# Performance work log

Measured on AMD Instinct MI355X. Metric: run time of the kernel, lower is better.

Reference implementation:

```python
import jax, jax.numpy as jnp
import numpy as np

B, S, D = 2, 2048, 2048
H, HD = 16, 128


def _rope_cos_sin(seq_len, head_dim, base=10000.0):
    inv_freq = 1.0 / (base ** (np.arange(0, head_dim, 2, dtype=np.float32) / head_dim))
    t = np.arange(seq_len, dtype=np.float32)
    freqs = np.outer(t, inv_freq)                      # [S, HD/2]
    emb = np.concatenate([freqs, freqs], axis=-1)      # [S, HD]
    return jnp.asarray(np.cos(emb)), jnp.asarray(np.sin(emb))


def setup_inputs() -> dict:
    key = jax.random.key(0)
    k1, k2, k3 = jax.random.split(key, 3)
    hidden_states = jax.random.normal(k1, (B, S, D), dtype=jnp.float32)
    cos, sin = _rope_cos_sin(S, HD)
    # qkv weight: [3, H*HD, D] as in CastedLinear(batch_output_dims=(3,))
    w_qkv = jax.random.normal(k2, (3, H * HD, D), dtype=jnp.float32) * (1.0 / D ** 0.5)
    w_o = jax.random.normal(k3, (D, H * HD), dtype=jnp.float32) * (1.0 / (H * HD) ** 0.5)
    return {"hidden_states": hidden_states, "cos": cos, "sin": sin, "w_qkv": w_qkv, "w_o": w_o}


def _rotate_half(x):
    x1, x2 = jnp.split(x, 2, axis=-1)
    return jnp.concatenate([-x2, x1], axis=-1)


def _apply_rope(x, cos, sin):
    # x: [B, S, H, HD]; cos/sin: [S, HD] -> broadcast over heads via [:, None, :]
    return x * cos[:, None, :] + _rotate_half(x) * sin[:, None, :]


def reference(hidden_states, cos, sin, w_qkv, w_o):
    # fused QKV projection: weight flattened to [3*H*HD, D]
    qkv = jnp.einsum('bsd,fd->bsf', hidden_states, w_qkv.reshape(-1, D))  # [B,S,3*H*HD]
    # rearrange '... (h hd) -> ... h hd' with h=H  ->  [B,S,H,3*HD], then chunk
    qkv = qkv.reshape(B, S, H, 3 * HD)
    q, k, v = jnp.split(qkv, 3, axis=-1)          # each [B,S,H,HD]
    q = _apply_rope(q, cos, sin)
    k = _apply_rope(k, cos, sin)
    # SDPA, causal
    scale = 1.0 / jnp.sqrt(jnp.asarray(HD, dtype=q.dtype))
    scores = jnp.einsum('bshd,bthd->bhst', q, k) * scale      # [B,H,S,S]
    causal = jnp.tril(jnp.ones((S, S), dtype=bool))
    scores = jnp.where(causal, scores, jnp.asarray(-jnp.inf, dtype=scores.dtype))
    probs = jax.nn.softmax(scores, axis=-1)
    attn = jnp.einsum('bhst,bthd->bshd', probs, v)            # [B,S,H,HD]
    attn = attn.reshape(B, S, H * HD)
    return jnp.einsum('bsf,df->bsd', attn, w_o)               # [B,S,D]
```

## Files before the change

kernel.cpp:

```cpp
#include <hip/hip_runtime.h>

typedef unsigned short u16;
typedef __bf16 bf16x8 __attribute__((ext_vector_type(8)));
typedef float f32x4 __attribute__((ext_vector_type(4)));


__device__ __forceinline__ u16 f2bf(float x) {
  __bf16 h = (__bf16)x;
  return __builtin_bit_cast(u16, h);
}

__device__ __forceinline__ void async_copy16(void* lds, const void* g) {
  __builtin_amdgcn_global_load_lds((const __attribute__((address_space(1))) void*)g,
                                   (__attribute__((address_space(3))) void*)lds, 16, 0, 0);
}

__global__ __launch_bounds__(256) void cast_all(const float* __restrict__ hidden,
                                                const float* __restrict__ wqkv,
                                                const float* __restrict__ wo,
                                                u16* __restrict__ xb,
                                                u16* __restrict__ wqb,
                                                u16* __restrict__ wob) {
  int i = blockIdx.x * 256 + threadIdx.x;
  const float* s;
  u16* d;
  int off;
  if (i < 2097152) { s = hidden; d = xb; off = i; }
  else if (i < 2097152 + 3145728) { s = wqkv; d = wqb; off = i - 2097152; }
  else { s = wo; d = wob; off = i - (2097152 + 3145728); }
  float4 v = ((const float4*)s)[off];
  ushort4 o;
  o.x = f2bf(v.x); o.y = f2bf(v.y); o.z = f2bf(v.z); o.w = f2bf(v.w);
  ((ushort4*)d)[off] = o;
}

__global__ __launch_bounds__(256) void gemm_qkv(const u16* __restrict__ A,
                                                const u16* __restrict__ W,
                                                const float* __restrict__ cosb,
                                                const float* __restrict__ sinb,
                                                u16* __restrict__ Qb,
                                                u16* __restrict__ Kb,
                                                u16* __restrict__ Vt) {
  __shared__ __align__(16) u16 As[128 * 64];
  __shared__ __align__(16) u16 Bs[128 * 64];
  const int tid = threadIdx.x;
  const int lane = tid & 63;
  const int wave = tid >> 6;
  const int wm = (wave >> 1) * 64;
  const int r16 = lane & 15;
  const int g4 = lane >> 4;
  const int rsw = r16 & 7;
  const int bm = blockIdx.x * 128;
  const int bn = blockIdx.y * 128;

  size_t aoff[4], boff[4];
  u16* ldsA[4];
  u16* ldsB[4];
#pragma unroll
  for (int i = 0; i < 4; i++) {
    int row = wave * 32 + i * 8 + (lane >> 3);
    int c = (lane & 7) ^ (row & 7);
    aoff[i] = (size_t)(bm + row) * 2048 + c * 8;
    boff[i] = (size_t)(bn + row) * 2048 + c * 8;
    ldsA[i] = &As[(wave * 4 + i) * 512];
    ldsB[i] = &Bs[(wave * 4 + i) * 512];
  }

  int bcol[4];
#pragma unroll
  for (int n = 0; n < 4; n++) bcol[n] = (wave & 1) * 32 + (n & 1) * 16 + (n >> 1) * 64;

  f32x4 acc[4][4];
  f32x4 zero = {0.0f, 0.0f, 0.0f, 0.0f};
#pragma unroll
  for (int m = 0; m < 4; m++)
#pragma unroll
    for (int n = 0; n < 4; n++) acc[m][n] = zero;

  for (int kt = 0; kt < 2048; kt += 64) {
    __syncthreads();
#pragma unroll
    for (int i = 0; i < 4; i++) {
      async_copy16(ldsA[i], A + aoff[i] + kt);
      async_copy16(ldsB[i], W + boff[i] + kt);
    }
    __syncthreads();
#pragma unroll
    for (int ks = 0; ks < 2; ks++) {
      bf16x8 af[4], bfr[4];
#pragma unroll
      for (int m = 0; m < 4; m++)
        af[m] = *(const bf16x8*)(&As[(wm + m * 16 + r16) * 64 + ((ks * 4 + g4) ^ rsw) * 8]);
#pragma unroll
      for (int n = 0; n < 4; n++)
        bfr[n] = *(const bf16x8*)(&Bs[(bcol[n] + r16) * 64 + ((ks * 4 + g4) ^ rsw) * 8]);
#pragma unroll
      for (int m = 0; m < 4; m++)
#pragma unroll
        for (int n = 0; n < 4; n++)
          acc[m][n] = __builtin_amdgcn_mfma_f32_16x16x32_bf16(af[m], bfr[n], acc[m][n], 0, 0, 0);
    }
  }

  const int which = blockIdx.y % 3;
  const int hh = blockIdx.y / 3;
  const float qs = (which == 0) ? 0.08838834764831845f * 1.4426950408889634f : 1.0f;
#pragma unroll
  for (int m = 0; m < 4; m++) {
#pragma unroll
    for (int r = 0; r < 4; r++) {
      int row = bm + wm + m * 16 + g4 * 4 + r;
      int bb = row >> 11;
      int s = row & 2047;
      size_t bhIdx = (size_t)(bb * 16 + hh);
      if (which == 2) {
#pragma unroll
        for (int n = 0; n < 4; n++) {
          int hd = bcol[n] + r16;
          Vt[(bhIdx * 128 + hd) * 2048 + s] = f2bf(acc[m][n][r]);
        }
      } else {
        u16* dst = (which ? Kb : Qb) + (bhIdx * 2048 + s) * 128;
#pragma unroll
        for (int n = 0; n < 2; n++) {
          int hd = bcol[n] + r16;
          float c = cosb[s * 128 + hd] * qs;
          float sn = sinb[s * 128 + hd] * qs;
          float x1 = acc[m][n][r], x2 = acc[m][n + 2][r];
          dst[hd] = f2bf(x1 * c - x2 * sn);
          dst[hd + 64] = f2bf(x2 * c + x1 * sn);
        }
      }
    }
  }
}

__global__ __launch_bounds__(256) void flash_attn(const u16* __restrict__ Q,
                                                  const u16* __restrict__ K,
                                                  const u16* __restrict__ Vt,
                                                  u16* __restrict__ O) {
  __shared__ __align__(16) u16 Ks[2][64 * 128];
  __shared__ __align__(16) u16 Vs[2][128 * 64];
  __shared__ __align__(16) u16 Ps[4 * 16 * 72];
  const int tid = threadIdx.x;
  const int lane = tid & 63;
  const int wave = tid >> 6;
  const int bh = blockIdx.y;
  const int r16 = lane & 15;
  const int g4 = lane >> 4;
  const int rsw = r16 & 7;
  const u16* Qh = Q + (size_t)bh * 2048 * 128;
  const u16* Kh = K + (size_t)bh * 2048 * 128;
  const u16* Vh = Vt + (size_t)bh * 128 * 2048;
  const int b = bh >> 4;
  const int h = bh & 15;

  size_t koff[4], voff[4];
  int ldsOff[4];
#pragma unroll
  for (int i = 0; i < 4; i++) {
    int kr = (wave * 4 + i) * 4 + (lane >> 4);
    int kc = (lane & 15) ^ (kr & 7);
    koff[i] = (size_t)kr * 128 + kc * 8;
    int vr = (wave * 4 + i) * 8 + (lane >> 3);
    int vc = (lane & 7) ^ (vr & 7);
    voff[i] = (size_t)vr * 2048 + vc * 8;
    ldsOff[i] = (wave * 4 + i) * 512;
  }

#pragma unroll 1
  for (int pass = 0; pass < 2; pass++) {
    const int t = pass == 0 ? (int)blockIdx.x : 31 - (int)blockIdx.x;

    bf16x8 qf[4];
    {
      int qrow = t * 64 + wave * 16 + r16;
#pragma unroll
      for (int ks = 0; ks < 4; ks++)
        qf[ks] = *(const bf16x8*)(Qh + (size_t)qrow * 128 + ks * 32 + g4 * 8);
    }

    f32x4 o[8];
    f32x4 zero = {0.0f, 0.0f, 0.0f, 0.0f};
#pragma unroll
    for (int c = 0; c < 8; c++) o[c] = zero;
    float m_i = -__builtin_inff();
    float l_i = 0.0f;

    __syncthreads();
#pragma unroll
    for (int i = 0; i < 4; i++) {
      async_copy16(&Ks[0][ldsOff[i]], Kh + koff[i]);
      async_copy16(&Vs[0][ldsOff[i]], Vh + voff[i]);
    }

    int cur = 0;
    for (int u = 0; u <= t; u++) {
      __syncthreads();
      if (u < t) {
#pragma unroll
        for (int i = 0; i < 4; i++) {
          async_copy16(&Ks[cur ^ 1][ldsOff[i]], Kh + (size_t)(u + 1) * 64 * 128 + koff[i]);
          async_copy16(&Vs[cur ^ 1][ldsOff[i]], Vh + (size_t)(u + 1) * 64 + voff[i]);
        }
      }

      f32x4 sacc[4];
#pragma unroll
      for (int n = 0; n < 4; n++) sacc[n] = zero;
#pragma unroll
      for (int n = 0; n < 4; n++) {
#pragma unroll
        for (int ks = 0; ks < 4; ks++) {
          bf16x8 kf = *(const bf16x8*)(&Ks[cur][(n * 16 + r16) * 128 + ((ks * 4 + g4) ^ rsw) * 8]);
          sacc[n] = __builtin_amdgcn_mfma_f32_16x16x32_bf16(kf, qf[ks], sacc[n], 0, 0, 0);
        }
      }

      const int qg = t * 64 + wave * 16 + r16;
      float e[4][4];
      float vmax = -__builtin_inff();
#pragma unroll
      for (int n = 0; n < 4; n++)
#pragma unroll
        for (int r = 0; r < 4; r++) {
          float ev = sacc[n][r];
          if (u == t) {
            int key = u * 64 + 16 * n + g4 * 4 + r;
            if (key > qg) ev = -__builtin_inff();
          }
          e[n][r] = ev;
          vmax = fmaxf(vmax, ev);
        }
      vmax = fmaxf(vmax, __shfl_xor(vmax, 16));
      vmax = fmaxf(vmax, __shfl_xor(vmax, 32));
      float mn = fmaxf(m_i, vmax);
      float alpha = exp2f(m_i - mn);
      m_i = mn;
      float ssum = 0.0f;
      u16* Pw = &Ps[wave * 16 * 72];
#pragma unroll
      for (int n = 0; n < 4; n++) {
        ushort4 pk;
        float p0 = exp2f(e[n][0] - mn);
        float p1 = exp2f(e[n][1] - mn);
        float p2 = exp2f(e[n][2] - mn);
        float p3 = exp2f(e[n][3] - mn);
        ssum += (p0 + p1) + (p2 + p3);
        pk.x = f2bf(p0); pk.y = f2bf(p1); pk.z = f2bf(p2); pk.w = f2bf(p3);
        *(ushort4*)(&Pw[r16 * 72 + 16 * n + g4 * 4]) = pk;
      }
      ssum += __shfl_xor(ssum, 16);
      ssum += __shfl_xor(ssum, 32);
      l_i = l_i * alpha + ssum;

#pragma unroll
      for (int c = 0; c < 8; c++)
#pragma unroll
        for (int r = 0; r < 4; r++) o[c][r] *= alpha;

#pragma unroll
      for (int ks2 = 0; ks2 < 2; ks2++) {
        bf16x8 pf = *(const bf16x8*)(&Pw[r16 * 72 + ks2 * 32 + g4 * 8]);
#pragma unroll
        for (int c = 0; c < 8; c++) {
          bf16x8 vf = *(const bf16x8*)(&Vs[cur][(c * 16 + r16) * 64 + ((ks2 * 4 + g4) ^ rsw) * 8]);
          o[c] = __builtin_amdgcn_mfma_f32_16x16x32_bf16(vf, pf, o[c], 0, 0, 0);
        }
      }
      cur ^= 1;
    }

    float rl = 1.0f / l_i;
    int srow = t * 64 + wave * 16 + r16;
    u16* dst = O + ((size_t)(b * 2048 + srow)) * 2048 + h * 128;
#pragma unroll
    for (int c = 0; c < 8; c++) {
      ushort4 pk;
      pk.x = f2bf(o[c][0] * rl);
      pk.y = f2bf(o[c][1] * rl);
      pk.z = f2bf(o[c][2] * rl);
      pk.w = f2bf(o[c][3] * rl);
      *(ushort4*)(dst + c * 16 + g4 * 4) = pk;
    }
  }
}

__global__ __launch_bounds__(256) void gemm_out(const u16* __restrict__ A,
                                                const u16* __restrict__ W,
                                                float* __restrict__ out) {
  __shared__ __align__(16) u16 As[128 * 64];
  __shared__ __align__(16) u16 Bs[128 * 64];
  const int tid = threadIdx.x;
  const int lane = tid & 63;
  const int wave = tid >> 6;
  const int wm = (wave >> 1) * 64;
  const int wn = (wave & 1) * 64;
  const int r16 = lane & 15;
  const int g4 = lane >> 4;
  const int rsw = r16 & 7;
  const int bm = blockIdx.x * 128;
  const int bn = blockIdx.y * 128;

  size_t aoff[4], boff[4];
  u16* ldsA[4];
  u16* ldsB[4];
#pragma unroll
  for (int i = 0; i < 4; i++) {
    int row = wave * 32 + i * 8 + (lane >> 3);
    int c = (lane & 7) ^ (row & 7);
    aoff[i] = (size_t)(bm + row) * 2048 + c * 8;
    boff[i] = (size_t)(bn + row) * 2048 + c * 8;
    ldsA[i] = &As[(wave * 4 + i) * 512];
    ldsB[i] = &Bs[(wave * 4 + i) * 512];
  }

  f32x4 acc[4][4];
  f32x4 zero = {0.0f, 0.0f, 0.0f, 0.0f};
#pragma unroll
  for (int m = 0; m < 4; m++)
#pragma unroll
    for (int n = 0; n < 4; n++) acc[m][n] = zero;

  for (int kt = 0; kt < 2048; kt += 64) {
    __syncthreads();
#pragma unroll
    for (int i = 0; i < 4; i++) {
      async_copy16(ldsA[i], A + aoff[i] + kt);
      async_copy16(ldsB[i], W + boff[i] + kt);
    }
    __syncthreads();
#pragma unroll
    for (int ks = 0; ks < 2; ks++) {
      bf16x8 af[4], bfr[4];
#pragma unroll
      for (int m = 0; m < 4; m++)
        af[m] = *(const bf16x8*)(&As[(wm + m * 16 + r16) * 64 + ((ks * 4 + g4) ^ rsw) * 8]);
#pragma unroll
      for (int n = 0; n < 4; n++)
        bfr[n] = *(const bf16x8*)(&Bs[(wn + n * 16 + r16) * 64 + ((ks * 4 + g4) ^ rsw) * 8]);
#pragma unroll
      for (int m = 0; m < 4; m++)
#pragma unroll
        for (int n = 0; n < 4; n++)
          acc[m][n] = __builtin_amdgcn_mfma_f32_16x16x32_bf16(af[m], bfr[n], acc[m][n], 0, 0, 0);
    }
  }

#pragma unroll
  for (int m = 0; m < 4; m++) {
#pragma unroll
    for (int n = 0; n < 4; n++) {
#pragma unroll
      for (int r = 0; r < 4; r++) {
        int row = bm + wm + m * 16 + g4 * 4 + r;
        int col = bn + wn + n * 16 + r16;
        out[(size_t)row * 2048 + col] = acc[m][n][r];
      }
    }
  }
}

extern "C" void kernel_launch(void* const* d_in, const int* in_sizes, int n_in,
                              void* d_out, int out_size, void* d_ws, size_t ws_size,
                              hipStream_t stream) {
  const float* hidden = (const float*)d_in[0];
  const float* cosb   = (const float*)d_in[1];
  const float* sinb   = (const float*)d_in[2];
  const float* w_qkv  = (const float*)d_in[3];
  const float* w_o    = (const float*)d_in[4];
  float* out = (float*)d_out;

  char* ws = (char*)d_ws;
  u16* Xbf    = (u16*)(ws);
  u16* Wqkvbf = (u16*)(ws + 16777216);
  u16* Wobf   = (u16*)(ws + 41943040);
  u16* Qb     = (u16*)(ws + 50331648);
  u16* Kb     = (u16*)(ws + 67108864);
  u16* Vt     = (u16*)(ws + 83886080);
  u16* Ob     = (u16*)(ws + 100663296);

  cast_all<<<24576, 256, 0, stream>>>(hidden, w_qkv, w_o, Xbf, Wqkvbf, Wobf);
  gemm_qkv<<<dim3(32, 48), 256, 0, stream>>>(Xbf, Wqkvbf, cosb, sinb, Qb, Kb, Vt);
  flash_attn<<<dim3(16, 32), 256, 0, stream>>>(Qb, Kb, Vt, Ob);
  gemm_out<<<dim3(32, 16), 256, 0, stream>>>(Ob, Wobf, out);
}
```

Measured before the change: 409.6 us.

## Use 128-key single-buffered KV tiles in flash attention instead of double-buffered 64

The flash attention kernel now processes 128 keys per iteration using the same LDS footprint, loading each K/V tile into one buffer between two barriers instead of prefetching the next 64-key tile into a second buffer. This halves the number of iterations and per-iteration softmax and rescale overhead, and the PV product is split into two halves that reuse the per-wave P scratch. In exchange, global loads no longer overlap with MFMA compute inside a block. The diagonal tile can now waste up to half its work on masked keys, and more score registers are live at once.

```diff
diff --git a/kernel.cpp b/kernel.cpp
--- a/kernel.cpp
+++ b/kernel.cpp
@@ -139,8 +139,8 @@
                                                   const u16* __restrict__ K,
                                                   const u16* __restrict__ Vt,
                                                   u16* __restrict__ O) {
-  __shared__ __align__(16) u16 Ks[2][64 * 128];
-  __shared__ __align__(16) u16 Vs[2][128 * 64];
+  __shared__ __align__(16) u16 Ks[128 * 128];
+  __shared__ __align__(16) u16 Vs[128 * 128];
   __shared__ __align__(16) u16 Ps[4 * 16 * 72];
   const int tid = threadIdx.x;
   const int lane = tid & 63;
@@ -155,30 +155,26 @@
   const int b = bh >> 4;
   const int h = bh & 15;
 
-  size_t koff[4], voff[4];
-  int ldsOff[4];
-#pragma unroll
-  for (int i = 0; i < 4; i++) {
-    int kr = (wave * 4 + i) * 4 + (lane >> 4);
-    int kc = (lane & 15) ^ (kr & 7);
-    koff[i] = (size_t)kr * 128 + kc * 8;
-    int vr = (wave * 4 + i) * 8 + (lane >> 3);
-    int vc = (lane & 7) ^ (vr & 7);
-    voff[i] = (size_t)vr * 2048 + vc * 8;
-    ldsOff[i] = (wave * 4 + i) * 512;
+  int koff[8], voff[8], ldsOff[8];
+#pragma unroll
+  for (int i = 0; i < 8; i++) {
+    int r = (wave * 8 + i) * 4 + (lane >> 4);
+    int c = (lane & 15) ^ (r & 7);
+    koff[i] = r * 128 + c * 8;
+    voff[i] = r * 2048 + c * 8;
+    ldsOff[i] = (wave * 8 + i) * 512;
   }
 
 #pragma unroll 1
   for (int pass = 0; pass < 2; pass++) {
     const int t = pass == 0 ? (int)blockIdx.x : 31 - (int)blockIdx.x;
+    const int qg = t * 64 + wave * 16 + r16;
+    const int nk = t / 2 + 1;
 
     bf16x8 qf[4];
-    {
-      int qrow = t * 64 + wave * 16 + r16;
-#pragma unroll
-      for (int ks = 0; ks < 4; ks++)
-        qf[ks] = *(const bf16x8*)(Qh + (size_t)qrow * 128 + ks * 32 + g4 * 8);
-    }
+#pragma unroll
+    for (int ks = 0; ks < 4; ks++)
+      qf[ks] = *(const bf16x8*)(Qh + (size_t)qg * 128 + ks * 32 + g4 * 8);
 
     f32x4 o[8];
     f32x4 zero = {0.0f, 0.0f, 0.0f, 0.0f};
@@ -187,93 +183,86 @@
     float m_i = -__builtin_inff();
     float l_i = 0.0f;
 
-    __syncthreads();
-#pragma unroll
-    for (int i = 0; i < 4; i++) {
-      async_copy16(&Ks[0][ldsOff[i]], Kh + koff[i]);
-      async_copy16(&Vs[0][ldsOff[i]], Vh + voff[i]);
-    }
-
-    int cur = 0;
-    for (int u = 0; u <= t; u++) {
+    for (int u = 0; u < nk; u++) {
       __syncthreads();
-      if (u < t) {
-#pragma unroll
-        for (int i = 0; i < 4; i++) {
-          async_copy16(&Ks[cur ^ 1][ldsOff[i]], Kh + (size_t)(u + 1) * 64 * 128 + koff[i]);
-          async_copy16(&Vs[cur ^ 1][ldsOff[i]], Vh + (size_t)(u + 1) * 64 + voff[i]);
-        }
-      }
-
-      f32x4 sacc[4];
-#pragma unroll
-      for (int n = 0; n < 4; n++) sacc[n] = zero;
-#pragma unroll
-      for (int n = 0; n < 4; n++) {
+#pragma unroll
+      for (int i = 0; i < 8; i++) {
+        async_copy16(&Ks[ldsOff[i]], Kh + (size_t)u * 16384 + koff[i]);
+        async_copy16(&Vs[ldsOff[i]], Vh + (size_t)u * 128 + voff[i]);
+      }
+      __syncthreads();
+
+      f32x4 sacc[8];
+#pragma unroll
+      for (int n = 0; n < 8; n++) sacc[n] = zero;
+#pragma unroll
+      for (int n = 0; n < 8; n++) {
 #pragma unroll
         for (int ks = 0; ks < 4; ks++) {
-          bf16x8 kf = *(const bf16x8*)(&Ks[cur][(n * 16 + r16) * 128 + ((ks * 4 + g4) ^ rsw) * 8]);
+          bf16x8 kf = *(const bf16x8*)(&Ks[(n * 16 + r16) * 128 + ((ks * 4 + g4) ^ rsw) * 8]);
           sacc[n] = __builtin_amdgcn_mfma_f32_16x16x32_bf16(kf, qf[ks], sacc[n], 0, 0, 0);
         }
       }
 
-      const int qg = t * 64 + wave * 16 + r16;
-      float e[4][4];
+      if (u == nk - 1) {
+#pragma unroll
+        for (int n = 0; n < 8; n++)
+#pragma unroll
+          for (int r = 0; r < 4; r++) {
+            int key = u * 128 + 16 * n + g4 * 4 + r;
+            if (key > qg) sacc[n][r] = -__builtin_inff();
+          }
+      }
       float vmax = -__builtin_inff();
 #pragma unroll
-      for (int n = 0; n < 4; n++)
-#pragma unroll
-        for (int r = 0; r < 4; r++) {
-          float ev = sacc[n][r];
-          if (u == t) {
-            int key = u * 64 + 16 * n + g4 * 4 + r;
-            if (key > qg) ev = -__builtin_inff();
-          }
-          e[n][r] = ev;
-          vmax = fmaxf(vmax, ev);
-        }
+      for (int n = 0; n < 8; n++)
+#pragma unroll
+        for (int r = 0; r < 4; r++) vmax = fmaxf(vmax, sacc[n][r]);
       vmax = fmaxf(vmax, __shfl_xor(vmax, 16));
       vmax = fmaxf(vmax, __shfl_xor(vmax, 32));
       float mn = fmaxf(m_i, vmax);
       float alpha = exp2f(m_i - mn);
       m_i = mn;
+
+#pragma unroll
+      for (int c = 0; c < 8; c++)
+#pragma unroll
+        for (int r = 0; r < 4; r++) o[c][r] *= alpha;
+
       float ssum = 0.0f;
       u16* Pw = &Ps[wave * 16 * 72];
 #pragma unroll
-      for (int n = 0; n < 4; n++) {
-        ushort4 pk;
-        float p0 = exp2f(e[n][0] - mn);
-        float p1 = exp2f(e[n][1] - mn);
-        float p2 = exp2f(e[n][2] - mn);
-        float p3 = exp2f(e[n][3] - mn);
-        ssum += (p0 + p1) + (p2 + p3);
-        pk.x = f2bf(p0); pk.y = f2bf(p1); pk.z = f2bf(p2); pk.w = f2bf(p3);
-        *(ushort4*)(&Pw[r16 * 72 + 16 * n + g4 * 4]) = pk;
+      for (int half = 0; half < 2; half++) {
+#pragma unroll
+        for (int nl = 0; nl < 4; nl++) {
+          int n = half * 4 + nl;
+          float p0 = exp2f(sacc[n][0] - mn);
+          float p1 = exp2f(sacc[n][1] - mn);
+          float p2 = exp2f(sacc[n][2] - mn);
+          float p3 = exp2f(sacc[n][3] - mn);
+          ssum += (p0 + p1) + (p2 + p3);
+          ushort4 pk;
+          pk.x = f2bf(p0); pk.y = f2bf(p1); pk.z = f2bf(p2); pk.w = f2bf(p3);
+          *(ushort4*)(&Pw[r16 * 72 + 16 * nl + g4 * 4]) = pk;
+        }
+#pragma unroll
+        for (int ks2 = 0; ks2 < 2; ks2++) {
+          bf16x8 pf = *(const bf16x8*)(&Pw[r16 * 72 + ks2 * 32 + g4 * 8]);
+          int kv = half * 2 + ks2;
+#pragma unroll
+          for (int c = 0; c < 8; c++) {
+            bf16x8 vf = *(const bf16x8*)(&Vs[(c * 16 + r16) * 128 + ((kv * 4 + g4) ^ rsw) * 8]);
+            o[c] = __builtin_amdgcn_mfma_f32_16x16x32_bf16(vf, pf, o[c], 0, 0, 0);
+          }
+        }
       }
       ssum += __shfl_xor(ssum, 16);
       ssum += __shfl_xor(ssum, 32);
       l_i = l_i * alpha + ssum;
-
-#pragma unroll
-      for (int c = 0; c < 8; c++)
-#pragma unroll
-        for (int r = 0; r < 4; r++) o[c][r] *= alpha;
-
-#pragma unroll
-      for (int ks2 = 0; ks2 < 2; ks2++) {
-        bf16x8 pf = *(const bf16x8*)(&Pw[r16 * 72 + ks2 * 32 + g4 * 8]);
-#pragma unroll
-        for (int c = 0; c < 8; c++) {
-          bf16x8 vf = *(const bf16x8*)(&Vs[cur][(c * 16 + r16) * 64 + ((ks2 * 4 + g4) ^ rsw) * 8]);
-          o[c] = __builtin_amdgcn_mfma_f32_16x16x32_bf16(vf, pf, o[c], 0, 0, 0);
-        }
-      }
-      cur ^= 1;
     }
 
     float rl = 1.0f / l_i;
-    int srow = t * 64 + wave * 16 + r16;
-    u16* dst = O + ((size_t)(b * 2048 + srow)) * 2048 + h * 128;
+    u16* dst = O + ((size_t)(b * 2048 + qg)) * 2048 + h * 128;
 #pragma unroll
     for (int c = 0; c < 8; c++) {
       ushort4 pk;
```

Result: no change. 409.7 us (+0.0%).
